# Kernel tuning notes

Hardware: AMD Instinct MI355X
Metric: run time of the kernel (lower is better)

## Reference

```python
import jax, jax.numpy as jnp
import numpy as np

B, C, H, W, MODES, RANK = 16, 128, 128, 128, 16, 8


def setup_inputs() -> dict:
    key = jax.random.key(0)
    ks = jax.random.split(key, 8)
    scale = 1.0 / (C * C)
    lr_scale = 0.02
    return {
        "x": jax.random.normal(ks[0], (B, C, H, W), dtype=jnp.float32),
        "w_real": scale * jax.random.normal(ks[1], (C, C, MODES, MODES), dtype=jnp.float32),
        "w_imag": scale * jax.random.normal(ks[2], (C, C, MODES, MODES), dtype=jnp.float32),
        "u_real": lr_scale * jax.random.normal(ks[3], (C, RANK, MODES, MODES), dtype=jnp.float32),
        "u_imag": lr_scale * jax.random.normal(ks[4], (C, RANK, MODES, MODES), dtype=jnp.float32),
        "v_real": lr_scale * jax.random.normal(ks[5], (C, RANK, MODES, MODES), dtype=jnp.float32),
        "v_imag": lr_scale * jax.random.normal(ks[6], (C, RANK, MODES, MODES), dtype=jnp.float32),
        "skip_w": (1.0 / np.sqrt(C)) * jax.random.normal(ks[7], (C, C), dtype=jnp.float32),
    }


def physical_act(x):
    # f(x) = x * exp(-|x|^2)
    return x * jnp.exp(-jnp.abs(x) ** 2)


def reference(x, w_real, w_imag, u_real, u_imag, v_real, v_imag, skip_w):
    Bb, Cc, Hh, Ww = x.shape
    # 1x1 conv skip path == channel matmul
    x_skip = jnp.einsum('oc,bchw->bohw', skip_w, x)
    # FFT to spectral domain: (B, C, H, W//2+1) complex64
    x_ft = jnp.fft.rfft2(x, norm='ortho')
    W_ft = x_ft.shape[-1]
    m1 = min(w_real.shape[-2], Hh)
    m2 = min(w_real.shape[-1], W_ft)
    # truncated-mode complex diagonal operator D (per-frequency channel mix)
    D = (w_real + 1j * w_imag)[:, :, :m1, :m2]          # (O, I, m1, m2)
    x_top = x_ft[:, :, :m1, :m2]                         # (B, I, m1, m2)
    out_top = jnp.einsum('bimn,oimn->bomn', x_top, D)
    # low-rank cross-frequency mixer UV*
    U = (u_real + 1j * u_imag)[:, :, :m1, :m2]           # (O, R, m1, m2)
    V = (v_real + 1j * v_imag)[:, :, :m1, :m2]           # (I, R, m1, m2)
    z = jnp.einsum('bimn,irmn->br', x_top, jnp.conj(V))  # (B, R)
    out_top = out_top + jnp.einsum('ormn,br->bomn', U, z)
    # scatter back into zero-padded full spectrum
    out_ft = jnp.zeros(x_ft.shape, dtype=x_ft.dtype).at[:, :, :m1, :m2].set(out_top)
    x_spectral = jnp.fft.irfft2(out_ft, s=(Hh, Ww), norm='ortho')
    out = x_spectral + x_skip
    return physical_act(out)
```

## Files before the change

kernel.cpp:

```cpp
#include <hip/hip_runtime.h>
#include <math.h>

#define TAB_OFF 0
#define XTOP_OFF 16384
#define Z_OFF (16384 + 1048576)
#define OTOP_OFF (Z_OFF + 256)
#define TF_OFF (OTOP_OFF + 1048576)
#define T2F_OFF (TF_OFF + 4096)
#define SWF_OFF XTOP_OFF


using bf16x8 = __attribute__((ext_vector_type(8))) short;
using s16x4  = __attribute__((ext_vector_type(4))) short;
using f32x16 = __attribute__((ext_vector_type(16))) float;

__device__ inline unsigned short bf_rnd(float v) {
  return (unsigned short)((__float_as_uint(v) + 0x8000u) >> 16);
}
__device__ inline void bf_split(float v, unsigned short& hi, unsigned short& lo) {
  unsigned u = __float_as_uint(v);
  hi = (unsigned short)(u >> 16);
  float r = v - __uint_as_float(u & 0xFFFF0000u);
  lo = (unsigned short)(__float_as_uint(r) >> 16);
}
__device__ inline bf16x8 ldfrag(const unsigned short* p) {
  s16x4 a = *(const s16x4*)p;
  s16x4 b = *(const s16x4*)(p + 4);
  bf16x8 r;
  r[0] = a[0]; r[1] = a[1]; r[2] = a[2]; r[3] = a[3];
  r[4] = b[0]; r[5] = b[1]; r[6] = b[2]; r[7] = b[3];
  return r;
}
__device__ inline bf16x8 ldfrag_sw(const unsigned short* base, int row, int koff) {
  int byte = row * 256 + ((koff * 2) ^ ((row & 7) << 4));
  return ldfrag((const unsigned short*)((const char*)base + byte));
}

__global__ __launch_bounds__(256) void k_tab(float* __restrict__ tab) {
  int idx = blockIdx.x * 256 + threadIdx.x;
  if (idx >= 16384) return;
  int which = idx >> 11, rem = idx & 2047;
  int a, j;
  if (which == 4 || which == 5) { a = rem & 127; j = rem >> 7; }
  else { a = rem >> 4; j = rem & 15; }
  int p = (a * j) & 127;
  float ang = (float)p * (float)(3.14159265358979323846 / 64.0);
  float cv = cosf(ang), sv = sinf(ang);
  float v;
  switch (which) {
    case 0: v = cv * (1.f / 128.f); break;
    case 1: v = -sv * (1.f / 128.f); break;
    case 2: v = cv; break;
    case 3: v = sv; break;
    case 4: v = cv; break;
    case 5: v = sv; break;
    case 6: v = ((rem & 15) == 0 ? 1.f : 2.f) * cv * (1.f / 128.f); break;
    default: v = ((rem & 15) == 0 ? 1.f : 2.f) * (-sv) * (1.f / 128.f); break;
  }
  tab[idx] = v;
}

__global__ __launch_bounds__(256) void k_fprep(unsigned short* __restrict__ tf) {
  int idx = blockIdx.x * 256 + threadIdx.x;
  if (idx >= 4096) return;
  int np = idx >> 7, k = idx & 127;
  int n = np & 15;
  int p = (k * n) & 127;
  float ang = (float)p * (float)(3.14159265358979323846 / 64.0);
  float v = (np < 16 ? cosf(ang) : -sinf(ang)) * (1.f / 128.f);
  unsigned short hi, lo;
  bf_split(v, hi, lo);
  tf[np * 128 + k] = hi;
  tf[4096 + np * 128 + k] = lo;
}

__global__ __launch_bounds__(256) void k_t2prep(const float* __restrict__ tab,
                                                unsigned short* __restrict__ t2f) {
  int idx = blockIdx.x * 256 + threadIdx.x;
  if (idx >= 4096) return;
  int w = idx >> 5, np = idx & 31;
  float v = (np < 16) ? tab[12288 + w * 16 + np] : tab[14336 + w * 16 + (np - 16)];
  t2f[idx] = bf_rnd(v);
}

__global__ __launch_bounds__(256) void k_wprep(const float* __restrict__ sw,
                                               unsigned short* __restrict__ swf) {
  int idx = blockIdx.x * 256 + threadIdx.x;
  if (idx >= 16384) return;
  int o = idx >> 7, k = idx & 127;
  unsigned short hb, lb;
  bf_split(sw[o * 128 + k], hb, lb);
  int kc = k >> 5, ks = (k >> 4) & 1, kh = (k >> 3) & 1, j = k & 7;
  int f0 = (kc * 2 + ks) * 2;
  swf[(f0 + 0) * 2048 + o * 16 + kh * 8 + j] = hb;
  swf[(f0 + 1) * 2048 + o * 16 + kh * 8 + j] = lb;
}

__global__ __launch_bounds__(256) void k_fwd(const float* __restrict__ x,
                                             const unsigned short* __restrict__ tf,
                                             const float* __restrict__ tab,
                                             float* __restrict__ xtop) {
  __shared__ unsigned short Xh[128 * 128];
  __shared__ unsigned short Tfh[32 * 128];
  __shared__ unsigned short Tfl[32 * 128];
  const int c = blockIdx.x, b = blockIdx.y;
  const int t = threadIdx.x;
  const int lane = t & 63, wv = t >> 6;

  #pragma unroll
  for (int it = 0; it < 32; ++it) {
    int idx = it * 256 + t;
    int part = idx >> 12, rem = idx & 4095;
    int row = rem >> 7, k = rem & 127;
    unsigned short v = tf[part * 4096 + rem];
    unsigned short* dst = part ? Tfl : Tfh;
    *(unsigned short*)((char*)dst + row * 256 + ((k * 2) ^ ((row & 7) << 4))) = v;
  }
  const float* img = x + (((size_t)(b * 128 + c)) << 14);
  #pragma unroll
  for (int it = 0; it < 16; ++it) {
    int flat = it * 256 + t;
    int h = flat >> 5, wq = flat & 31;
    float4 v = *(const float4*)(img + (size_t)flat * 4);
    s16x4 pk;
    pk[0] = (short)bf_rnd(v.x); pk[1] = (short)bf_rnd(v.y);
    pk[2] = (short)bf_rnd(v.z); pk[3] = (short)bf_rnd(v.w);
    *(s16x4*)((char*)Xh + h * 256 + ((wq * 8) ^ ((h & 7) << 4))) = pk;
  }
  __syncthreads();

  f32x16 acc;
  #pragma unroll
  for (int e = 0; e < 16; ++e) acc[e] = 0.f;
  const int orow = wv * 32 + (lane & 31);
  const int bcol = lane & 31;
  const int kh8 = (lane >> 5) * 8;
  #pragma unroll
  for (int kc8 = 0; kc8 < 8; ++kc8) {
    int kfull = kc8 * 16 + kh8;
    bf16x8 a  = ldfrag_sw(Xh, orow, kfull);
    bf16x8 th = ldfrag_sw(Tfh, bcol, kfull);
    bf16x8 tl = ldfrag_sw(Tfl, bcol, kfull);
    acc = __builtin_amdgcn_mfma_f32_32x32x16_bf16(a, th, acc, 0, 0, 0);
    acc = __builtin_amdgcn_mfma_f32_32x32x16_bf16(a, tl, acc, 0, 0, 0);
  }
  __syncthreads();

  float* Arp = (float*)Xh;
  float* Aip = Arp + 16 * 132;
  {
    const int col = lane & 31;
    #pragma unroll
    for (int r = 0; r < 16; ++r) {
      int h = wv * 32 + (r & 3) + 8 * (r >> 2) + 4 * (lane >> 5);
      if (col < 16) Arp[col * 132 + h] = acc[r];
      else          Aip[(col - 16) * 132 + h] = acc[r];
    }
  }
  __syncthreads();

  {
    const int m = t >> 4, n = t & 15;
    const float* tc = tab + 8192 + m * 128;
    const float* ts = tab + 10240 + m * 128;
    const float* ar = Arp + n * 132;
    const float* ai = Aip + n * 132;
    float xr = 0.f, xi = 0.f;
    #pragma unroll 8
    for (int h4 = 0; h4 < 128; h4 += 4) {
      float4 av = *(const float4*)(ar + h4);
      float4 iv = *(const float4*)(ai + h4);
      float4 cv = *(const float4*)(tc + h4);
      float4 sv = *(const float4*)(ts + h4);
      xr += av.x * cv.x + iv.x * sv.x;  xi += iv.x * cv.x - av.x * sv.x;
      xr += av.y * cv.y + iv.y * sv.y;  xi += iv.y * cv.y - av.y * sv.y;
      xr += av.z * cv.z + iv.z * sv.z;  xi += iv.z * cv.z - av.z * sv.z;
      xr += av.w * cv.w + iv.w * sv.w;  xi += iv.w * cv.w - av.w * sv.w;
    }
    size_t base = ((size_t)(b * 128 + c)) * 512 + (size_t)(m * 16 + n) * 2;
    xtop[base] = xr; xtop[base + 1] = xi;
  }
}

__global__ __launch_bounds__(256) void k_z(const float* __restrict__ xtop,
                                           const float* __restrict__ vre,
                                           const float* __restrict__ vim,
                                           float* __restrict__ zout) {
  int b = blockIdx.x, ic = blockIdx.y, t = threadIdx.x;
  float zr[8], zi[8];
  #pragma unroll
  for (int r = 0; r < 8; ++r) { zr[r] = 0.f; zi[r] = 0.f; }
  const float* xb = xtop + ((size_t)b * 128) * 512;
  for (int i = ic * 16; i < ic * 16 + 16; ++i) {
    float xr = xb[i * 512 + t * 2], xi = xb[i * 512 + t * 2 + 1];
    #pragma unroll
    for (int r = 0; r < 8; ++r) {
      float vr = vre[(size_t)(i * 8 + r) * 256 + t];
      float vi = vim[(size_t)(i * 8 + r) * 256 + t];
      zr[r] += xr * vr + xi * vi;
      zi[r] += xi * vr - xr * vi;
    }
  }
  #pragma unroll
  for (int r = 0; r < 8; ++r)
    for (int off = 32; off > 0; off >>= 1) {
      zr[r] += __shfl_down(zr[r], off);
      zi[r] += __shfl_down(zi[r], off);
    }
  __shared__ float red[4][16];
  int wid = t >> 6, lane = t & 63;
  if (lane == 0) {
    #pragma unroll
    for (int r = 0; r < 8; ++r) { red[wid][r * 2] = zr[r]; red[wid][r * 2 + 1] = zi[r]; }
  }
  __syncthreads();
  if (t < 16) atomicAdd(&zout[b * 16 + t], red[0][t] + red[1][t] + red[2][t] + red[3][t]);
}

__global__ __launch_bounds__(256) void k_mix(const float* __restrict__ xtop,
                                             const float* __restrict__ wre,
                                             const float* __restrict__ wim,
                                             const float* __restrict__ ure,
                                             const float* __restrict__ uim,
                                             const float* __restrict__ z,
                                             float* __restrict__ otop) {
  int o0 = blockIdx.x * 4, b0 = blockIdx.y * 2, ic = blockIdx.z, t = threadIdx.x;
  float ar[2][4], ai[2][4];
  #pragma unroll
  for (int bb = 0; bb < 2; ++bb)
    #pragma unroll
    for (int oo = 0; oo < 4; ++oo) { ar[bb][oo] = 0.f; ai[bb][oo] = 0.f; }
  const float* x0 = xtop + ((size_t)(b0 * 128)) * 512;
  const float* x1 = x0 + 128 * 512;
  for (int i = ic * 16; i < ic * 16 + 16; ++i) {
    float x0r = x0[i * 512 + t * 2], x0i = x0[i * 512 + t * 2 + 1];
    float x1r = x1[i * 512 + t * 2], x1i = x1[i * 512 + t * 2 + 1];
    #pragma unroll
    for (int oo = 0; oo < 4; ++oo) {
      size_t di = (size_t)((o0 + oo) * 128 + i) * 256 + t;
      float dr = wre[di], dj = wim[di];
      ar[0][oo] += dr * x0r - dj * x0i; ai[0][oo] += dr * x0i + dj * x0r;
      ar[1][oo] += dr * x1r - dj * x1i; ai[1][oo] += dr * x1i + dj * x1r;
    }
  }
  if (ic == 0) {
    float zr[2][8], zi[2][8];
    #pragma unroll
    for (int bb = 0; bb < 2; ++bb)
      #pragma unroll
      for (int r = 0; r < 8; ++r) {
        zr[bb][r] = z[(b0 + bb) * 16 + r * 2];
        zi[bb][r] = z[(b0 + bb) * 16 + r * 2 + 1];
      }
    #pragma unroll
    for (int oo = 0; oo < 4; ++oo)
      #pragma unroll
      for (int r = 0; r < 8; ++r) {
        float urv = ure[(size_t)((o0 + oo) * 8 + r) * 256 + t];
        float uiv = uim[(size_t)((o0 + oo) * 8 + r) * 256 + t];
        #pragma unroll
        for (int bb = 0; bb < 2; ++bb) {
          ar[bb][oo] += urv * zr[bb][r] - uiv * zi[bb][r];
          ai[bb][oo] += urv * zi[bb][r] + uiv * zr[bb][r];
        }
      }
  }
  #pragma unroll
  for (int bb = 0; bb < 2; ++bb)
    #pragma unroll
    for (int oo = 0; oo < 4; ++oo) {
      size_t oi = ((size_t)((b0 + bb) * 128 + o0 + oo) * 256 + (size_t)t) * 2;
      atomicAdd(&otop[oi], ar[bb][oo]);
      atomicAdd(&otop[oi + 1], ai[bb][oo]);
    }
}

__global__ __launch_bounds__(256) void k_out(const float* __restrict__ x,
                                             const unsigned short* __restrict__ swf,
                                             const unsigned short* __restrict__ t2f,
                                             const float* __restrict__ otop,
                                             const float* __restrict__ tab,
                                             float* __restrict__ out) {
  __shared__ unsigned short Ylds[128 * 36];
  const int h = blockIdx.x, b = blockIdx.y;
  const int t = threadIdx.x;
  const int lane = t & 63, wv = t >> 6;
  const int kh8 = (lane >> 5) * 8;
  const int col = lane & 31;
  const int w0 = wv * 32;

  {
    int o = t >> 1, nh = (t & 1) * 8;
    float yr[8], yi[8];
    #pragma unroll
    for (int j = 0; j < 8; ++j) { yr[j] = 0.f; yi[j] = 0.f; }
    const float* xb = otop + ((size_t)(b * 128 + o)) * 512 + nh * 2;
    #pragma unroll 4
    for (int m = 0; m < 16; ++m) {
      float cm = tab[4096 + h * 16 + m];
      float sm = tab[6144 + h * 16 + m];
      float4 q0 = *(const float4*)(xb + m * 32 + 0);
      float4 q1 = *(const float4*)(xb + m * 32 + 4);
      float4 q2 = *(const float4*)(xb + m * 32 + 8);
      float4 q3 = *(const float4*)(xb + m * 32 + 12);
      yr[0] += q0.x * cm - q0.y * sm; yi[0] += q0.x * sm + q0.y * cm;
      yr[1] += q0.z * cm - q0.w * sm; yi[1] += q0.z * sm + q0.w * cm;
      yr[2] += q1.x * cm - q1.y * sm; yi[2] += q1.x * sm + q1.y * cm;
      yr[3] += q1.z * cm - q1.w * sm; yi[3] += q1.z * sm + q1.w * cm;
      yr[4] += q2.x * cm - q2.y * sm; yi[4] += q2.x * sm + q2.y * cm;
      yr[5] += q2.z * cm - q2.w * sm; yi[5] += q2.z * sm + q2.w * cm;
      yr[6] += q3.x * cm - q3.y * sm; yi[6] += q3.x * sm + q3.y * cm;
      yr[7] += q3.z * cm - q3.w * sm; yi[7] += q3.z * sm + q3.w * cm;
    }
    #pragma unroll
    for (int j = 0; j < 8; ++j) {
      Ylds[o * 36 + nh + j] = bf_rnd(yr[j]);
      Ylds[o * 36 + 16 + nh + j] = bf_rnd(yi[j]);
    }
  }
  __syncthreads();

  f32x16 acc[4];
  #pragma unroll
  for (int ot = 0; ot < 4; ++ot)
    #pragma unroll
    for (int e = 0; e < 16; ++e) acc[ot][e] = 0.f;

  const float* xb = x + (size_t)b * 2097152 + (size_t)h * 128 + (w0 + col);
  #pragma unroll
  for (int ks8 = 0; ks8 < 8; ++ks8) {
    const int c0 = ks8 * 16 + kh8;
    float xd[8];
    #pragma unroll
    for (int j = 0; j < 8; ++j) xd[j] = xb[(size_t)(c0 + j) * 16384];
    bf16x8 bh, bl;
    #pragma unroll
    for (int j = 0; j < 8; ++j) {
      unsigned short hb, lb;
      bf_split(xd[j], hb, lb);
      bh[j] = (short)hb; bl[j] = (short)lb;
    }
    const unsigned short* abase = swf + ks8 * 4096 + kh8;
    #pragma unroll
    for (int ot = 0; ot < 4; ++ot) {
      const int o = ot * 32 + col;
      bf16x8 ah = *(const bf16x8*)(abase + o * 16);
      bf16x8 al = *(const bf16x8*)(abase + 2048 + o * 16);
      acc[ot] = __builtin_amdgcn_mfma_f32_32x32x16_bf16(ah, bh, acc[ot], 0, 0, 0);
      acc[ot] = __builtin_amdgcn_mfma_f32_32x32x16_bf16(ah, bl, acc[ot], 0, 0, 0);
      acc[ot] = __builtin_amdgcn_mfma_f32_32x32x16_bf16(al, bh, acc[ot], 0, 0, 0);
    }
  }

  #pragma unroll
  for (int ks = 0; ks < 2; ++ks) {
    const int kb = ks * 16 + kh8;
    bf16x8 tb = *(const bf16x8*)(t2f + (w0 + col) * 32 + kb);
    #pragma unroll
    for (int ot = 0; ot < 4; ++ot) {
      bf16x8 ya = ldfrag(&Ylds[(ot * 32 + col) * 36 + kb]);
      acc[ot] = __builtin_amdgcn_mfma_f32_32x32x16_bf16(ya, tb, acc[ot], 0, 0, 0);
    }
  }

  #pragma unroll
  for (int ot = 0; ot < 4; ++ot) {
    #pragma unroll
    for (int r = 0; r < 16; ++r) {
      int o = ot * 32 + (r & 3) + 8 * (r >> 2) + 4 * (lane >> 5);
      float v = acc[ot][r];
      out[((size_t)(b * 128 + o)) * 16384 + (size_t)h * 128 + w0 + col] = v * __expf(-v * v);
    }
  }
}

extern "C" void kernel_launch(void* const* d_in, const int* in_sizes, int n_in,
                              void* d_out, int out_size, void* d_ws, size_t ws_size,
                              hipStream_t stream) {
  const float* x  = (const float*)d_in[0];
  const float* wr = (const float*)d_in[1];
  const float* wi = (const float*)d_in[2];
  const float* ur = (const float*)d_in[3];
  const float* ui = (const float*)d_in[4];
  const float* vr = (const float*)d_in[5];
  const float* vi = (const float*)d_in[6];
  const float* sw = (const float*)d_in[7];
  float* out  = (float*)d_out;
  float* ws   = (float*)d_ws;
  float* tab  = ws + TAB_OFF;
  float* xtop = ws + XTOP_OFF;
  float* z    = ws + Z_OFF;
  float* otop = ws + OTOP_OFF;
  unsigned short* tf  = (unsigned short*)(ws + TF_OFF);
  unsigned short* t2f = (unsigned short*)(ws + T2F_OFF);
  unsigned short* swf = (unsigned short*)(ws + SWF_OFF);

  hipMemsetAsync(z, 0, 256 * sizeof(float), stream);
  hipMemsetAsync(otop, 0, 1048576 * sizeof(float), stream);
  hipLaunchKernelGGL(k_tab, dim3(64), dim3(256), 0, stream, tab);
  hipLaunchKernelGGL(k_fprep, dim3(16), dim3(256), 0, stream, tf);
  hipLaunchKernelGGL(k_t2prep, dim3(16), dim3(256), 0, stream, tab, t2f);
  hipLaunchKernelGGL(k_fwd, dim3(128, 16), dim3(256), 0, stream, x, tf, tab, xtop);
  hipLaunchKernelGGL(k_z,   dim3(16, 8), dim3(256), 0, stream, xtop, vr, vi, z);
  hipLaunchKernelGGL(k_mix, dim3(32, 8, 8), dim3(256), 0, stream, xtop, wr, wi, ur, ui, z, otop);
  hipLaunchKernelGGL(k_wprep, dim3(64), dim3(256), 0, stream, sw, swf);
  hipLaunchKernelGGL(k_out, dim3(128, 16), dim3(256), 0, stream, x, swf, t2f, otop, tab, out);
}
```

Measured before the change: 207.6 us.

## Precompute inverse H-DFT spectrum into bf16 workspace via separate kernel

```diff
diff --git a/kernel.cpp b/kernel.cpp
--- a/kernel.cpp
+++ b/kernel.cpp
@@ -7,6 +7,8 @@
 #define OTOP_OFF (Z_OFF + 256)
 #define TF_OFF (OTOP_OFF + 1048576)
 #define T2F_OFF (TF_OFF + 4096)
+#define YF_OFF (T2F_OFF + 2048)
+#define YF_FLOATS 4194304
 #define SWF_OFF XTOP_OFF
 
 
@@ -275,12 +277,119 @@
     }
 }
 
-__global__ __launch_bounds__(256) void k_out(const float* __restrict__ x,
-                                             const unsigned short* __restrict__ swf,
-                                             const unsigned short* __restrict__ t2f,
-                                             const float* __restrict__ otop,
-                                             const float* __restrict__ tab,
-                                             float* __restrict__ out) {
+__global__ __launch_bounds__(256) void k_y(const float* __restrict__ otop,
+                                           const float* __restrict__ tab,
+                                           unsigned short* __restrict__ yf) {
+  const int b = blockIdx.x, oc = blockIdx.y, hc = blockIdx.z;
+  const int t = threadIdx.x;
+  const int part = t >> 7;
+  const int o = oc * 16 + ((t >> 3) & 15);
+  const int j0 = t & 7;
+  float xr0[16], xi0[16], xr1[16], xi1[16];
+  const float* xb = otop + ((size_t)(b * 128 + o)) * 512 + j0 * 4;
+  #pragma unroll
+  for (int m = 0; m < 16; ++m) {
+    float4 q = *(const float4*)(xb + m * 32);
+    xr0[m] = q.x; xi0[m] = q.y; xr1[m] = q.z; xi1[m] = q.w;
+  }
+  unsigned short* dst = yf + ((size_t)(b * 128) * 128 + o) * 32 + part * 16 + j0 * 2;
+  const float* tc = tab + 4096;
+  const float* ts = tab + 6144;
+  for (int h = hc * 64; h < hc * 64 + 64; ++h) {
+    float a0 = 0.f, a1 = 0.f;
+    if (part == 0) {
+      #pragma unroll
+      for (int m = 0; m < 16; ++m) {
+        float cm = tc[h * 16 + m], sm = ts[h * 16 + m];
+        a0 += xr0[m] * cm - xi0[m] * sm;
+        a1 += xr1[m] * cm - xi1[m] * sm;
+      }
+    } else {
+      #pragma unroll
+      for (int m = 0; m < 16; ++m) {
+        float cm = tc[h * 16 + m], sm = ts[h * 16 + m];
+        a0 += xr0[m] * sm + xi0[m] * cm;
+        a1 += xr1[m] * sm + xi1[m] * cm;
+      }
+    }
+    ushort2 pk; pk.x = bf_rnd(a0); pk.y = bf_rnd(a1);
+    *(ushort2*)(dst + (size_t)h * 4096) = pk;
+  }
+}
+
+__global__ __launch_bounds__(256) void k_out_y(const float* __restrict__ x,
+                                               const unsigned short* __restrict__ swf,
+                                               const unsigned short* __restrict__ t2f,
+                                               const unsigned short* __restrict__ yf,
+                                               float* __restrict__ out) {
+  const int h = blockIdx.x, b = blockIdx.y;
+  const int t = threadIdx.x;
+  const int lane = t & 63, wv = t >> 6;
+  const int kh8 = (lane >> 5) * 8;
+  const int col = lane & 31;
+  const int w0 = wv * 32;
+
+  f32x16 acc[4];
+  #pragma unroll
+  for (int ot = 0; ot < 4; ++ot)
+    #pragma unroll
+    for (int e = 0; e < 16; ++e) acc[ot][e] = 0.f;
+
+  const float* xb = x + (size_t)b * 2097152 + (size_t)h * 128 + (w0 + col);
+  #pragma unroll
+  for (int ks8 = 0; ks8 < 8; ++ks8) {
+    const int c0 = ks8 * 16 + kh8;
+    float xd[8];
+    #pragma unroll
+    for (int j = 0; j < 8; ++j) xd[j] = xb[(size_t)(c0 + j) * 16384];
+    bf16x8 bh, bl;
+    #pragma unroll
+    for (int j = 0; j < 8; ++j) {
+      unsigned short hb, lb;
+      bf_split(xd[j], hb, lb);
+      bh[j] = (short)hb; bl[j] = (short)lb;
+    }
+    const unsigned short* abase = swf + ks8 * 4096 + kh8;
+    #pragma unroll
+    for (int ot = 0; ot < 4; ++ot) {
+      const int o = ot * 32 + col;
+      bf16x8 ah = *(const bf16x8*)(abase + o * 16);
+      bf16x8 al = *(const bf16x8*)(abase + 2048 + o * 16);
+      acc[ot] = __builtin_amdgcn_mfma_f32_32x32x16_bf16(ah, bh, acc[ot], 0, 0, 0);
+      acc[ot] = __builtin_amdgcn_mfma_f32_32x32x16_bf16(ah, bl, acc[ot], 0, 0, 0);
+      acc[ot] = __builtin_amdgcn_mfma_f32_32x32x16_bf16(al, bh, acc[ot], 0, 0, 0);
+    }
+  }
+
+  const unsigned short* yb = yf + (size_t)(b * 128 + h) * 4096;
+  #pragma unroll
+  for (int ks = 0; ks < 2; ++ks) {
+    const int kb = ks * 16 + kh8;
+    bf16x8 tb = *(const bf16x8*)(t2f + (w0 + col) * 32 + kb);
+    #pragma unroll
+    for (int ot = 0; ot < 4; ++ot) {
+      bf16x8 ya = *(const bf16x8*)(yb + (ot * 32 + col) * 32 + kb);
+      acc[ot] = __builtin_amdgcn_mfma_f32_32x32x16_bf16(ya, tb, acc[ot], 0, 0, 0);
+    }
+  }
+
+  #pragma unroll
+  for (int ot = 0; ot < 4; ++ot) {
+    #pragma unroll
+    for (int r = 0; r < 16; ++r) {
+      int o = ot * 32 + (r & 3) + 8 * (r >> 2) + 4 * (lane >> 5);
+      float v = acc[ot][r];
+      out[((size_t)(b * 128 + o)) * 16384 + (size_t)h * 128 + w0 + col] = v * __expf(-v * v);
+    }
+  }
+}
+
+__global__ __launch_bounds__(256) void k_out_fb(const float* __restrict__ x,
+                                                const unsigned short* __restrict__ swf,
+                                                const unsigned short* __restrict__ t2f,
+                                                const float* __restrict__ otop,
+                                                const float* __restrict__ tab,
+                                                float* __restrict__ out) {
   __shared__ unsigned short Ylds[128 * 36];
   const int h = blockIdx.x, b = blockIdx.y;
   const int t = threadIdx.x;
@@ -394,6 +503,9 @@
   unsigned short* tf  = (unsigned short*)(ws + TF_OFF);
   unsigned short* t2f = (unsigned short*)(ws + T2F_OFF);
   unsigned short* swf = (unsigned short*)(ws + SWF_OFF);
+  unsigned short* yf  = (unsigned short*)(ws + YF_OFF);
+
+  const bool big_ws = ws_size >= (size_t)(YF_OFF + YF_FLOATS) * sizeof(float);
 
   hipMemsetAsync(z, 0, 256 * sizeof(float), stream);
   hipMemsetAsync(otop, 0, 1048576 * sizeof(float), stream);
@@ -404,5 +516,10 @@
   hipLaunchKernelGGL(k_z,   dim3(16, 8), dim3(256), 0, stream, xtop, vr, vi, z);
   hipLaunchKernelGGL(k_mix, dim3(32, 8, 8), dim3(256), 0, stream, xtop, wr, wi, ur, ui, z, otop);
   hipLaunchKernelGGL(k_wprep, dim3(64), dim3(256), 0, stream, sw, swf);
-  hipLaunchKernelGGL(k_out, dim3(128, 16), dim3(256), 0, stream, x, swf, t2f, otop, tab, out);
-}
+  if (big_ws) {
+    hipLaunchKernelGGL(k_y, dim3(16, 8, 2), dim3(256), 0, stream, otop, tab, yf);
+    hipLaunchKernelGGL(k_out_y, dim3(128, 16), dim3(256), 0, stream, x, swf, t2f, yf, out);
+  } else {
+    hipLaunchKernelGGL(k_out_fb, dim3(128, 16), dim3(256), 0, stream, x, swf, t2f, otop, tab, out);
+  }
+}
```

New measurement: 225.4 us. 1.09x slower.
